# Kernel optimization log

Hardware: AMD Instinct MI355X
Metric: run time of the kernel (lower is better)

## Reference

```python
import jax, jax.numpy as jnp
import numpy as np

ALPHA = 0.2  # LeakyReLU negative slope (init arg `alpha`)
N, F_IN, F_OUT = 8192, 512, 256


def setup_inputs() -> dict:
    key = jax.random.key(0)
    k1, k2, k3, k4 = jax.random.split(key, 4)
    x = jax.random.normal(k1, (N, F_IN), dtype=jnp.float32)
    adj = jax.random.randint(k2, (N, N), 0, 2, dtype=jnp.int32)
    W = jax.random.normal(k3, (F_IN, F_OUT), dtype=jnp.float32) * (1.0 / np.sqrt(F_IN))
    a = jax.random.normal(k4, (2 * F_OUT, 1), dtype=jnp.float32) * (1.0 / np.sqrt(F_IN))
    return {"x": x, "adj": adj, "W": W, "a": a}


def reference(x, adj, W, a):
    h = x @ W  # [N, F_OUT]
    f_out = W.shape[1]
    # e[i,j] = LeakyReLU(a1 . h_i + a2 . h_j); computed without the O(N^2*2F) concat
    f1 = h @ a[:f_out, 0]   # [N]
    f2 = h @ a[f_out:, 0]   # [N]
    s = f1[:, None] + f2[None, :]  # [N, N]
    e = jnp.where(s >= 0, s, ALPHA * s)
    # Faithful to the source bug: -9e15 * zeros_like == zeros, so masked entries are 0.0
    att = jnp.where(adj > 0, e, jnp.zeros((), dtype=e.dtype))
    att = jax.nn.softmax(att, axis=1)
    # dropout is identity in eval mode
    h_prime = att @ h  # [N, F_OUT]
    return jax.nn.elu(h_prime)  # concat=True branch
```

## Files before the change

### kernel.cpp

```cpp
#include <hip/hip_runtime.h>
#include <stdint.h>

#define NN 8192
#define FIN 512
#define FOUT 256
#define ALPHA 0.2f
#define KSPLIT 4

typedef float f32x4 __attribute__((ext_vector_type(4)));
typedef short s16x8 __attribute__((ext_vector_type(8)));

__device__ __forceinline__ uint16_t f2bf(float f) {
  union { float f; uint32_t u; } v; v.f = f;
  uint32_t u = v.u + 0x7fffu + ((v.u >> 16) & 1u);
  return (uint16_t)(u >> 16);
}

__global__ __launch_bounds__(256) void k_wa(const float* __restrict__ W,
                                            const float* __restrict__ a,
                                            float* __restrict__ wa1, float* __restrict__ wa2) {
  __shared__ float a1[256], a2[256];
  int tid = threadIdx.x;
  a1[tid] = a[tid];
  a2[tid] = a[tid + 256];
  __syncthreads();
  int m = blockIdx.x * 256 + tid;
  const float* wrow = W + (size_t)m * FOUT;
  float s1 = 0.f, s2 = 0.f;
  for (int k = 0; k < FOUT; k += 4) {
    f32x4 v = *(const f32x4*)(wrow + k);
#pragma unroll
    for (int i = 0; i < 4; i++) {
      s1 += v[i] * a1[k + i];
      s2 += v[i] * a2[k + i];
    }
  }
  wa1[m] = s1; wa2[m] = s2;
}

__global__ __launch_bounds__(256) void k_f1f2(const float* __restrict__ x,
                                              const float* __restrict__ wa1,
                                              const float* __restrict__ wa2,
                                              float* __restrict__ f1, float* __restrict__ f2) {
  __shared__ float s1[512], s2[512];
  int tid = threadIdx.x;
  s1[tid] = wa1[tid]; s1[tid + 256] = wa1[tid + 256];
  s2[tid] = wa2[tid]; s2[tid + 256] = wa2[tid + 256];
  __syncthreads();
  int w = tid >> 6, l = tid & 63;
  int row = blockIdx.x * 4 + w;
  const float* xr = x + (size_t)row * FIN + l * 8;
  f32x4 v0 = *(const f32x4*)xr;
  f32x4 v1 = *(const f32x4*)(xr + 4);
  int kb = l * 8;
  float d1 = 0.f, d2 = 0.f;
#pragma unroll
  for (int i = 0; i < 4; i++) {
    d1 += v0[i] * s1[kb + i] + v1[i] * s1[kb + 4 + i];
    d2 += v0[i] * s2[kb + i] + v1[i] * s2[kb + 4 + i];
  }
#pragma unroll
  for (int off = 32; off; off >>= 1) {
    d1 += __shfl_down(d1, off);
    d2 += __shfl_down(d2, off);
  }
  if (l == 0) { f1[row] = d1; f2[row] = d2; }
}

__global__ __launch_bounds__(256) void k_prep_wt(const float* __restrict__ W,
                                                 uint16_t* __restrict__ wt) {
  int idx = blockIdx.x * 256 + threadIdx.x;
  int f  = idx >> 7;
  int k4 = (idx & 127) * 4;
  ushort4 o;
  o.x = f2bf(W[(size_t)(k4 + 0) * FOUT + f]);
  o.y = f2bf(W[(size_t)(k4 + 1) * FOUT + f]);
  o.z = f2bf(W[(size_t)(k4 + 2) * FOUT + f]);
  o.w = f2bf(W[(size_t)(k4 + 3) * FOUT + f]);
  *(ushort4*)(wt + (size_t)f * FIN + k4) = o;
}

__global__ __launch_bounds__(256, 2) void k_gemm_h(const float* __restrict__ x,
                                                   const uint16_t* __restrict__ wt,
                                                   uint16_t* __restrict__ h) {
  __shared__ uint16_t Xs[64][40];
  __shared__ uint16_t Ws[128][40];
  int i0 = blockIdx.x * 64;
  int f0 = blockIdx.y * 128;
  int tid = threadIdx.x;
  int w = tid >> 6, l = tid & 63;
  int wr = w >> 1, wc = w & 1;
  int q = l >> 4, r16 = l & 15;
  f32x4 acc[2][4];
#pragma unroll
  for (int a = 0; a < 2; a++)
#pragma unroll
    for (int b = 0; b < 4; b++) acc[a][b] = (f32x4)0.f;

  int srow = tid >> 2, sch = tid & 3;
  for (int k0 = 0; k0 < FIN; k0 += 32) {
    const float* xp = x + (size_t)(i0 + srow) * FIN + k0 + sch * 8;
    f32x4 u0 = *(const f32x4*)xp;
    f32x4 u1 = *(const f32x4*)(xp + 4);
    uint4 pk;
    pk.x = (uint32_t)f2bf(u0[0]) | ((uint32_t)f2bf(u0[1]) << 16);
    pk.y = (uint32_t)f2bf(u0[2]) | ((uint32_t)f2bf(u0[3]) << 16);
    pk.z = (uint32_t)f2bf(u1[0]) | ((uint32_t)f2bf(u1[1]) << 16);
    pk.w = (uint32_t)f2bf(u1[2]) | ((uint32_t)f2bf(u1[3]) << 16);
    *(uint4*)(&Xs[srow][sch * 8]) = pk;
#pragma unroll
    for (int r = 0; r < 2; r++) {
      int idx = tid + r * 256;
      int rr = idx >> 2, cc = idx & 3;
      uint4 vw = *(const uint4*)(wt + (size_t)(f0 + rr) * FIN + k0 + cc * 8);
      *(uint4*)(&Ws[rr][cc * 8]) = vw;
    }
    __syncthreads();
    s16x8 A[2], B[4];
#pragma unroll
    for (int a = 0; a < 2; a++) A[a] = *(const s16x8*)(&Xs[wr * 32 + a * 16 + r16][q * 8]);
#pragma unroll
    for (int b = 0; b < 4; b++) B[b] = *(const s16x8*)(&Ws[wc * 64 + b * 16 + r16][q * 8]);
#pragma unroll
    for (int a = 0; a < 2; a++)
#pragma unroll
      for (int b = 0; b < 4; b++)
        acc[a][b] = __builtin_amdgcn_mfma_f32_16x16x32_bf16(A[a], B[b], acc[a][b], 0, 0, 0);
    __syncthreads();
  }
#pragma unroll
  for (int a = 0; a < 2; a++)
#pragma unroll
    for (int b = 0; b < 4; b++)
#pragma unroll
      for (int reg = 0; reg < 4; reg++) {
        int row = i0 + wr * 32 + a * 16 + q * 4 + reg;
        int col = f0 + wc * 64 + b * 16 + r16;
        h[(size_t)row * FOUT + col] = f2bf(acc[a][b][reg]);
      }
}

__global__ __launch_bounds__(256) void k_transpose(const uint16_t* __restrict__ h,
                                                   uint16_t* __restrict__ ht) {
  __shared__ uint16_t T[64][72];
  int i0 = blockIdx.x * 64, f0 = blockIdx.y * 64;
  int tid = threadIdx.x;
#pragma unroll
  for (int p = 0; p < 2; p++) {
    int idx = tid + p * 256;
    int r = idx >> 3, c8 = idx & 7;
    uint4 v = *(const uint4*)(h + (size_t)(i0 + r) * FOUT + f0 + c8 * 8);
    *(uint4*)(&T[r][c8 * 8]) = v;
  }
  __syncthreads();
#pragma unroll
  for (int p = 0; p < 2; p++) {
    int idx = tid + p * 256;
    int fr = idx >> 3, ic8 = idx & 7;
    s16x8 v;
#pragma unroll
    for (int j = 0; j < 8; j++) v[j] = (short)T[ic8 * 8 + j][fr];
    *(s16x8*)(ht + (size_t)(f0 + fr) * NN + i0 + ic8 * 8) = v;
  }
}

__global__ __launch_bounds__(256) void k_zero(float* __restrict__ l_arr) {
  l_arr[blockIdx.x * 256 + threadIdx.x] = 0.f;
}

__global__ __launch_bounds__(256, 2) void k_att(const int* __restrict__ adj,
                                                const uint16_t* __restrict__ ht,
                                                const float* __restrict__ f1,
                                                const float* __restrict__ f2,
                                                float* __restrict__ l_arr,
                                                float* __restrict__ part) {
  __shared__ uint16_t Ps[64][40];
  __shared__ uint16_t Hs[256][40];
  int i0 = blockIdx.x * 64;
  int jbase = blockIdx.y * (NN / KSPLIT);
  int tid = threadIdx.x;
  int w = tid >> 6, l = tid & 63;
  int q = l >> 4, r16 = l & 15;
  int prow = tid >> 2, pch = tid & 3;
  float f1i = f1[i0 + prow];
  float lsum = 0.f;
  f32x4 acc[4][4];
#pragma unroll
  for (int a = 0; a < 4; a++)
#pragma unroll
    for (int b = 0; b < 4; b++) acc[a][b] = (f32x4)0.f;

  for (int s = 0; s < NN / KSPLIT; s += 32) {
    int j0 = jbase + s;
#pragma unroll
    for (int p = 0; p < 4; p++) {
      int idx = tid + p * 256;
      int hr = idx >> 2, hc = idx & 3;
      uint4 v = *(const uint4*)(ht + (size_t)hr * NN + j0 + hc * 8);
      *(uint4*)(&Hs[hr][hc * 8]) = v;
    }
    const int* ap = adj + (size_t)(i0 + prow) * NN + j0 + pch * 8;
    int4 A0 = *(const int4*)ap;
    int4 A1 = *(const int4*)(ap + 4);
    f32x4 F0 = *(const f32x4*)(f2 + j0 + pch * 8);
    f32x4 F1 = *(const f32x4*)(f2 + j0 + pch * 8 + 4);
    s16x8 pv;
#define PCOMP(Ac, Fc, kk) { float s_ = f1i + (Fc); float e_ = s_ > 0.f ? s_ : ALPHA * s_; \
                            float p_ = ((Ac) != 0) ? __expf(e_) : 1.0f; lsum += p_; \
                            pv[kk] = (short)f2bf(p_); }
    PCOMP(A0.x, F0[0], 0); PCOMP(A0.y, F0[1], 1); PCOMP(A0.z, F0[2], 2); PCOMP(A0.w, F0[3], 3);
    PCOMP(A1.x, F1[0], 4); PCOMP(A1.y, F1[1], 5); PCOMP(A1.z, F1[2], 6); PCOMP(A1.w, F1[3], 7);
#undef PCOMP
    *(s16x8*)(&Ps[prow][pch * 8]) = pv;
    __syncthreads();

    s16x8 Af[4], Bf[4];
#pragma unroll
    for (int a = 0; a < 4; a++) Af[a] = *(const s16x8*)(&Ps[a * 16 + r16][q * 8]);
#pragma unroll
    for (int b = 0; b < 4; b++) Bf[b] = *(const s16x8*)(&Hs[w * 64 + b * 16 + r16][q * 8]);
#pragma unroll
    for (int a = 0; a < 4; a++)
#pragma unroll
      for (int b = 0; b < 4; b++)
        acc[a][b] = __builtin_amdgcn_mfma_f32_16x16x32_bf16(Af[a], Bf[b], acc[a][b], 0, 0, 0);
    __syncthreads();
  }

  lsum += __shfl_down(lsum, 2);
  lsum += __shfl_down(lsum, 1);
  if (pch == 0) atomicAdd(&l_arr[i0 + prow], lsum);

  float* pb = part + (size_t)blockIdx.y * ((size_t)NN * FOUT);
#pragma unroll
  for (int a = 0; a < 4; a++)
#pragma unroll
    for (int b = 0; b < 4; b++)
#pragma unroll
      for (int reg = 0; reg < 4; reg++) {
        int row = i0 + a * 16 + q * 4 + reg;
        int col = w * 64 + b * 16 + r16;
        pb[(size_t)row * FOUT + col] = acc[a][b][reg];
      }
}

__global__ __launch_bounds__(256) void k_combine(const float* __restrict__ part,
                                                 const float* __restrict__ l_arr,
                                                 float* __restrict__ out) {
  int idx = (blockIdx.x * 256 + threadIdx.x) * 4;
  float r = 1.0f / l_arr[idx >> 8];
  f32x4 v0 = *(const f32x4*)(part + 0 * (size_t)(NN * FOUT) + idx);
  f32x4 v1 = *(const f32x4*)(part + 1 * (size_t)(NN * FOUT) + idx);
  f32x4 v2 = *(const f32x4*)(part + 2 * (size_t)(NN * FOUT) + idx);
  f32x4 v3 = *(const f32x4*)(part + 3 * (size_t)(NN * FOUT) + idx);
  f32x4 o;
#pragma unroll
  for (int i = 0; i < 4; i++) {
    float v = (v0[i] + v1[i] + v2[i] + v3[i]) * r;
    o[i] = v > 0.f ? v : (__expf(v) - 1.f);
  }
  *(f32x4*)(out + idx) = o;
}

extern "C" void kernel_launch(void* const* d_in, const int* in_sizes, int n_in,
                              void* d_out, int out_size, void* d_ws, size_t ws_size,
                              hipStream_t stream) {
  const float* x   = (const float*)d_in[0];
  const int*   adj = (const int*)d_in[1];
  const float* W   = (const float*)d_in[2];
  const float* a   = (const float*)d_in[3];
  float* out = (float*)d_out;

  char* ws = (char*)d_ws;
  float*    wa1   = (float*)ws;
  float*    wa2   = wa1 + 512;
  float*    f1    = wa2 + 512;
  float*    f2    = f1 + NN;
  float*    l_arr = f2 + NN;
  uint16_t* wt    = (uint16_t*)(l_arr + NN);
  uint16_t* h     = wt + (size_t)FOUT * FIN;
  uint16_t* ht    = h + (size_t)NN * FOUT;
  float*    part  = (float*)(ht + (size_t)NN * FOUT);

  k_wa<<<2, 256, 0, stream>>>(W, a, wa1, wa2);
  k_f1f2<<<NN / 4, 256, 0, stream>>>(x, wa1, wa2, f1, f2);
  k_prep_wt<<<128, 256, 0, stream>>>(W, wt);
  k_gemm_h<<<dim3(NN / 64, 2), 256, 0, stream>>>(x, wt, h);
  k_transpose<<<dim3(NN / 64, FOUT / 64), 256, 0, stream>>>(h, ht);
  k_zero<<<NN / 256, 256, 0, stream>>>(l_arr);
  k_att<<<dim3(NN / 64, KSPLIT), 256, 0, stream>>>(adj, ht, f1, f2, l_arr, part);
  k_combine<<<NN * FOUT / 1024, 256, 0, stream>>>(part, l_arr, out);
}
```

Before: 458.4 us.

## Fuse transpose into GEMM epilogue and register-prefetch tiles in attention kernel

The h GEMM now writes its output directly in transposed layout, which removes the separate transpose kernel and the intermediate h buffer. Both the GEMM and the attention kernel move to 512-thread blocks (8 waves) with a smaller per-wave accumulator tile. Each loop iteration prefetches the next tile's global loads into registers to overlap memory latency with MFMA work. The attention kernel also stages its f2 slice in shared memory once. The transposed epilogue uses strided 8-byte stores, and the larger blocks raise register and LDS pressure per block.

```diff
diff --git a/kernel.cpp b/kernel.cpp
--- a/kernel.cpp
+++ b/kernel.cpp
@@ -6,9 +6,12 @@
 #define FOUT 256
 #define ALPHA 0.2f
 #define KSPLIT 4
+#define KSLICE (NN / KSPLIT)
+#define BK 32
 
 typedef float f32x4 __attribute__((ext_vector_type(4)));
 typedef short s16x8 __attribute__((ext_vector_type(8)));
+typedef short s16x4 __attribute__((ext_vector_type(4)));
 
 __device__ __forceinline__ uint16_t f2bf(float f) {
   union { float f; uint32_t u; } v; v.f = f;
@@ -80,166 +83,162 @@
   *(ushort4*)(wt + (size_t)f * FIN + k4) = o;
 }
 
-__global__ __launch_bounds__(256, 2) void k_gemm_h(const float* __restrict__ x,
+__global__ __launch_bounds__(512, 4) void k_gemm_h(const float* __restrict__ x,
                                                    const uint16_t* __restrict__ wt,
-                                                   uint16_t* __restrict__ h) {
-  __shared__ uint16_t Xs[64][40];
-  __shared__ uint16_t Ws[128][40];
+                                                   uint16_t* __restrict__ ht) {
+  __shared__ __align__(16) uint16_t Xs[64][40];
+  __shared__ __align__(16) uint16_t Ws[256][40];
   int i0 = blockIdx.x * 64;
-  int f0 = blockIdx.y * 128;
-  int tid = threadIdx.x;
-  int w = tid >> 6, l = tid & 63;
-  int wr = w >> 1, wc = w & 1;
+  int tid = threadIdx.x;
+  int l = tid & 63, w = tid >> 6;
   int q = l >> 4, r16 = l & 15;
-  f32x4 acc[2][4];
-#pragma unroll
-  for (int a = 0; a < 2; a++)
-#pragma unroll
-    for (int b = 0; b < 4; b++) acc[a][b] = (f32x4)0.f;
-
-  int srow = tid >> 2, sch = tid & 3;
-  for (int k0 = 0; k0 < FIN; k0 += 32) {
-    const float* xp = x + (size_t)(i0 + srow) * FIN + k0 + sch * 8;
-    f32x4 u0 = *(const f32x4*)xp;
-    f32x4 u1 = *(const f32x4*)(xp + 4);
-    uint4 pk;
-    pk.x = (uint32_t)f2bf(u0[0]) | ((uint32_t)f2bf(u0[1]) << 16);
-    pk.y = (uint32_t)f2bf(u0[2]) | ((uint32_t)f2bf(u0[3]) << 16);
-    pk.z = (uint32_t)f2bf(u1[0]) | ((uint32_t)f2bf(u1[1]) << 16);
-    pk.w = (uint32_t)f2bf(u1[2]) | ((uint32_t)f2bf(u1[3]) << 16);
-    *(uint4*)(&Xs[srow][sch * 8]) = pk;
-#pragma unroll
-    for (int r = 0; r < 2; r++) {
-      int idx = tid + r * 256;
-      int rr = idx >> 2, cc = idx & 3;
-      uint4 vw = *(const uint4*)(wt + (size_t)(f0 + rr) * FIN + k0 + cc * 8);
-      *(uint4*)(&Ws[rr][cc * 8]) = vw;
+  f32x4 acc[4][2];
+#pragma unroll
+  for (int a = 0; a < 4; a++)
+#pragma unroll
+    for (int b = 0; b < 2; b++) acc[a][b] = (f32x4)0.f;
+
+  int xr = tid >> 3, xc = (tid & 7) * 4;
+  int wr = tid >> 1, wc = (tid & 1) * 16;
+  const float* xp = x + (size_t)(i0 + xr) * FIN + xc;
+  const uint16_t* wp = wt + (size_t)wr * FIN + wc;
+
+  f32x4 xv = *(const f32x4*)xp;
+  uint4 wA = *(const uint4*)wp;
+  uint4 wB = *(const uint4*)(wp + 8);
+
+  const int ITERS = FIN / BK;
+  for (int s = 0; s < ITERS; s++) {
+    int sn = (s + 1 < ITERS) ? (s + 1) : s;
+    f32x4 xv2 = *(const f32x4*)(xp + sn * BK);
+    uint4 wA2 = *(const uint4*)(wp + sn * BK);
+    uint4 wB2 = *(const uint4*)(wp + sn * BK + 8);
+
+    s16x4 xb;
+#pragma unroll
+    for (int i = 0; i < 4; i++) xb[i] = (short)f2bf(xv[i]);
+    *(s16x4*)(&Xs[xr][xc]) = xb;
+    *(uint4*)(&Ws[wr][wc]) = wA;
+    *(uint4*)(&Ws[wr][wc + 8]) = wB;
+    __syncthreads();
+
+    s16x8 Af[4], Bf[2];
+#pragma unroll
+    for (int a = 0; a < 4; a++) Af[a] = *(const s16x8*)(&Xs[a * 16 + r16][q * 8]);
+#pragma unroll
+    for (int b = 0; b < 2; b++) Bf[b] = *(const s16x8*)(&Ws[w * 32 + b * 16 + r16][q * 8]);
+#pragma unroll
+    for (int a = 0; a < 4; a++)
+#pragma unroll
+      for (int b = 0; b < 2; b++)
+        acc[a][b] = __builtin_amdgcn_mfma_f32_16x16x32_bf16(Af[a], Bf[b], acc[a][b], 0, 0, 0);
+    __syncthreads();
+    xv = xv2; wA = wA2; wB = wB2;
+  }
+
+#pragma unroll
+  for (int a = 0; a < 4; a++)
+#pragma unroll
+    for (int b = 0; b < 2; b++) {
+      int f = w * 32 + b * 16 + r16;
+      int i = i0 + a * 16 + q * 4;
+      ushort4 o;
+      o.x = f2bf(acc[a][b][0]); o.y = f2bf(acc[a][b][1]);
+      o.z = f2bf(acc[a][b][2]); o.w = f2bf(acc[a][b][3]);
+      *(ushort4*)(ht + (size_t)f * NN + i) = o;
     }
-    __syncthreads();
-    s16x8 A[2], B[4];
-#pragma unroll
-    for (int a = 0; a < 2; a++) A[a] = *(const s16x8*)(&Xs[wr * 32 + a * 16 + r16][q * 8]);
-#pragma unroll
-    for (int b = 0; b < 4; b++) B[b] = *(const s16x8*)(&Ws[wc * 64 + b * 16 + r16][q * 8]);
-#pragma unroll
-    for (int a = 0; a < 2; a++)
-#pragma unroll
-      for (int b = 0; b < 4; b++)
-        acc[a][b] = __builtin_amdgcn_mfma_f32_16x16x32_bf16(A[a], B[b], acc[a][b], 0, 0, 0);
-    __syncthreads();
-  }
-#pragma unroll
-  for (int a = 0; a < 2; a++)
-#pragma unroll
-    for (int b = 0; b < 4; b++)
-#pragma unroll
-      for (int reg = 0; reg < 4; reg++) {
-        int row = i0 + wr * 32 + a * 16 + q * 4 + reg;
-        int col = f0 + wc * 64 + b * 16 + r16;
-        h[(size_t)row * FOUT + col] = f2bf(acc[a][b][reg]);
-      }
-}
-
-__global__ __launch_bounds__(256) void k_transpose(const uint16_t* __restrict__ h,
-                                                   uint16_t* __restrict__ ht) {
-  __shared__ uint16_t T[64][72];
-  int i0 = blockIdx.x * 64, f0 = blockIdx.y * 64;
-  int tid = threadIdx.x;
-#pragma unroll
-  for (int p = 0; p < 2; p++) {
-    int idx = tid + p * 256;
-    int r = idx >> 3, c8 = idx & 7;
-    uint4 v = *(const uint4*)(h + (size_t)(i0 + r) * FOUT + f0 + c8 * 8);
-    *(uint4*)(&T[r][c8 * 8]) = v;
-  }
-  __syncthreads();
-#pragma unroll
-  for (int p = 0; p < 2; p++) {
-    int idx = tid + p * 256;
-    int fr = idx >> 3, ic8 = idx & 7;
-    s16x8 v;
-#pragma unroll
-    for (int j = 0; j < 8; j++) v[j] = (short)T[ic8 * 8 + j][fr];
-    *(s16x8*)(ht + (size_t)(f0 + fr) * NN + i0 + ic8 * 8) = v;
-  }
 }
 
 __global__ __launch_bounds__(256) void k_zero(float* __restrict__ l_arr) {
   l_arr[blockIdx.x * 256 + threadIdx.x] = 0.f;
 }
 
-__global__ __launch_bounds__(256, 2) void k_att(const int* __restrict__ adj,
+__global__ __launch_bounds__(512, 4) void k_att(const int* __restrict__ adj,
                                                 const uint16_t* __restrict__ ht,
                                                 const float* __restrict__ f1,
                                                 const float* __restrict__ f2,
                                                 float* __restrict__ l_arr,
                                                 float* __restrict__ part) {
-  __shared__ uint16_t Ps[64][40];
-  __shared__ uint16_t Hs[256][40];
+  __shared__ __align__(16) uint16_t Ps[64][40];
+  __shared__ __align__(16) uint16_t Hs[256][40];
+  __shared__ __align__(16) float Fs[KSLICE];
   int i0 = blockIdx.x * 64;
-  int jbase = blockIdx.y * (NN / KSPLIT);
-  int tid = threadIdx.x;
-  int w = tid >> 6, l = tid & 63;
+  int jbase = blockIdx.y * KSLICE;
+  int tid = threadIdx.x;
+  int l = tid & 63, w = tid >> 6;
   int q = l >> 4, r16 = l & 15;
-  int prow = tid >> 2, pch = tid & 3;
-  float f1i = f1[i0 + prow];
+  int pr = tid >> 3, pc = tid & 7;
+  int hr = tid >> 1, hc = (tid & 1) * 16;
+
+  *(f32x4*)(&Fs[tid * 4]) = *(const f32x4*)(f2 + jbase + tid * 4);
+
+  float f1i = f1[i0 + pr];
   float lsum = 0.f;
-  f32x4 acc[4][4];
-#pragma unroll
-  for (int a = 0; a < 4; a++)
-#pragma unroll
-    for (int b = 0; b < 4; b++) acc[a][b] = (f32x4)0.f;
-
-  for (int s = 0; s < NN / KSPLIT; s += 32) {
-    int j0 = jbase + s;
-#pragma unroll
-    for (int p = 0; p < 4; p++) {
-      int idx = tid + p * 256;
-      int hr = idx >> 2, hc = idx & 3;
-      uint4 v = *(const uint4*)(ht + (size_t)hr * NN + j0 + hc * 8);
-      *(uint4*)(&Hs[hr][hc * 8]) = v;
+  f32x4 acc[4][2];
+#pragma unroll
+  for (int a = 0; a < 4; a++)
+#pragma unroll
+    for (int b = 0; b < 2; b++) acc[a][b] = (f32x4)0.f;
+
+  const int* adjp = adj + (size_t)(i0 + pr) * NN + jbase + pc * 4;
+  const uint16_t* htp = ht + (size_t)hr * NN + jbase + hc;
+
+  int4 adjR = *(const int4*)adjp;
+  uint4 hA = *(const uint4*)htp;
+  uint4 hB = *(const uint4*)(htp + 8);
+  __syncthreads();
+
+  const int ITERS = KSLICE / BK;
+  for (int s = 0; s < ITERS; s++) {
+    int sn = (s + 1 < ITERS) ? (s + 1) : s;
+    int4 adjN = *(const int4*)(adjp + (size_t)sn * BK);
+    uint4 hA2 = *(const uint4*)(htp + sn * BK);
+    uint4 hB2 = *(const uint4*)(htp + sn * BK + 8);
+
+    f32x4 F = *(const f32x4*)(&Fs[s * BK + pc * 4]);
+    s16x4 pv;
+#pragma unroll
+    for (int i = 0; i < 4; i++) {
+      float s_ = f1i + F[i];
+      float e_ = fmaxf(s_, ALPHA * s_);
+      int av = (i == 0) ? adjR.x : (i == 1) ? adjR.y : (i == 2) ? adjR.z : adjR.w;
+      float p_ = (av != 0) ? __expf(e_) : 1.0f;
+      lsum += p_;
+      pv[i] = (short)f2bf(p_);
     }
-    const int* ap = adj + (size_t)(i0 + prow) * NN + j0 + pch * 8;
-    int4 A0 = *(const int4*)ap;
-    int4 A1 = *(const int4*)(ap + 4);
-    f32x4 F0 = *(const f32x4*)(f2 + j0 + pch * 8);
-    f32x4 F1 = *(const f32x4*)(f2 + j0 + pch * 8 + 4);
-    s16x8 pv;
-#define PCOMP(Ac, Fc, kk) { float s_ = f1i + (Fc); float e_ = s_ > 0.f ? s_ : ALPHA * s_; \
-                            float p_ = ((Ac) != 0) ? __expf(e_) : 1.0f; lsum += p_; \
-                            pv[kk] = (short)f2bf(p_); }
-    PCOMP(A0.x, F0[0], 0); PCOMP(A0.y, F0[1], 1); PCOMP(A0.z, F0[2], 2); PCOMP(A0.w, F0[3], 3);
-    PCOMP(A1.x, F1[0], 4); PCOMP(A1.y, F1[1], 5); PCOMP(A1.z, F1[2], 6); PCOMP(A1.w, F1[3], 7);
-#undef PCOMP
-    *(s16x8*)(&Ps[prow][pch * 8]) = pv;
-    __syncthreads();
-
-    s16x8 Af[4], Bf[4];
+    *(s16x4*)(&Ps[pr][pc * 4]) = pv;
+    *(uint4*)(&Hs[hr][hc]) = hA;
+    *(uint4*)(&Hs[hr][hc + 8]) = hB;
+    __syncthreads();
+
+    s16x8 Af[4], Bf[2];
 #pragma unroll
     for (int a = 0; a < 4; a++) Af[a] = *(const s16x8*)(&Ps[a * 16 + r16][q * 8]);
 #pragma unroll
-    for (int b = 0; b < 4; b++) Bf[b] = *(const s16x8*)(&Hs[w * 64 + b * 16 + r16][q * 8]);
+    for (int b = 0; b < 2; b++) Bf[b] = *(const s16x8*)(&Hs[w * 32 + b * 16 + r16][q * 8]);
 #pragma unroll
     for (int a = 0; a < 4; a++)
 #pragma unroll
-      for (int b = 0; b < 4; b++)
+      for (int b = 0; b < 2; b++)
         acc[a][b] = __builtin_amdgcn_mfma_f32_16x16x32_bf16(Af[a], Bf[b], acc[a][b], 0, 0, 0);
     __syncthreads();
-  }
-
+    adjR = adjN; hA = hA2; hB = hB2;
+  }
+
+  lsum += __shfl_down(lsum, 4);
   lsum += __shfl_down(lsum, 2);
   lsum += __shfl_down(lsum, 1);
-  if (pch == 0) atomicAdd(&l_arr[i0 + prow], lsum);
+  if (pc == 0) atomicAdd(&l_arr[i0 + pr], lsum);
 
   float* pb = part + (size_t)blockIdx.y * ((size_t)NN * FOUT);
 #pragma unroll
   for (int a = 0; a < 4; a++)
 #pragma unroll
-    for (int b = 0; b < 4; b++)
+    for (int b = 0; b < 2; b++)
 #pragma unroll
       for (int reg = 0; reg < 4; reg++) {
         int row = i0 + a * 16 + q * 4 + reg;
-        int col = w * 64 + b * 16 + r16;
+        int col = w * 32 + b * 16 + r16;
         pb[(size_t)row * FOUT + col] = acc[a][b][reg];
       }
 }
@@ -278,16 +277,14 @@
   float*    f2    = f1 + NN;
   float*    l_arr = f2 + NN;
   uint16_t* wt    = (uint16_t*)(l_arr + NN);
-  uint16_t* h     = wt + (size_t)FOUT * FIN;
-  uint16_t* ht    = h + (size_t)NN * FOUT;
+  uint16_t* ht    = wt + (size_t)FOUT * FIN;
   float*    part  = (float*)(ht + (size_t)NN * FOUT);
 
   k_wa<<<2, 256, 0, stream>>>(W, a, wa1, wa2);
   k_f1f2<<<NN / 4, 256, 0, stream>>>(x, wa1, wa2, f1, f2);
   k_prep_wt<<<128, 256, 0, stream>>>(W, wt);
-  k_gemm_h<<<dim3(NN / 64, 2), 256, 0, stream>>>(x, wt, h);
-  k_transpose<<<dim3(NN / 64, FOUT / 64), 256, 0, stream>>>(h, ht);
+  k_gemm_h<<<128, 512, 0, stream>>>(x, wt, ht);
   k_zero<<<NN / 256, 256, 0, stream>>>(l_arr);
-  k_att<<<dim3(NN / 64, KSPLIT), 256, 0, stream>>>(adj, ht, f1, f2, l_arr, part);
+  k_att<<<dim3(NN / 64, KSPLIT), 512, 0, stream>>>(adj, ht, f1, f2, l_arr, part);
   k_combine<<<NN * FOUT / 1024, 256, 0, stream>>>(part, l_arr, out);
 }
```

New measurement: 473.6 us. 3.3% more time.
